# Optimization experiments

Hardware: AMD Instinct MI355X
Metric: run time of the kernel (lower is better)

## Reference

```python
import jax, jax.numpy as jnp
import numpy as np

D_MODEL = 2048
NUM_HEADS = 32
NUM_KV_HEADS = 8
D_K = D_MODEL // NUM_HEADS
B, S = 2, 2048


def setup_inputs() -> dict:
    key = jax.random.key(0)
    ks = jax.random.split(key, 6)
    sc = 1.0 / np.sqrt(D_MODEL)
    x = jax.random.normal(ks[0], (B, S, D_MODEL), dtype=jnp.float32)
    mask = jnp.tril(jnp.ones((S, S), dtype=jnp.float32))[None, None]  # [1,1,S,S]
    return {
        'x': x,
        'mask': mask,
        'Wq': jax.random.normal(ks[1], (D_MODEL, D_MODEL), jnp.float32) * sc,
        'bq': jnp.zeros((D_MODEL,), jnp.float32),
        'Wk': jax.random.normal(ks[2], (D_MODEL, NUM_KV_HEADS * D_K), jnp.float32) * sc,
        'bk': jnp.zeros((NUM_KV_HEADS * D_K,), jnp.float32),
        'Wv': jax.random.normal(ks[3], (D_MODEL, NUM_KV_HEADS * D_K), jnp.float32) * sc,
        'bv': jnp.zeros((NUM_KV_HEADS * D_K,), jnp.float32),
        'Wo': jax.random.normal(ks[4], (D_MODEL, D_MODEL), jnp.float32) * sc,
        'bo': jnp.zeros((D_MODEL,), jnp.float32),
    }


def reference(x, mask, Wq, bq, Wk, bk, Wv, bv, Wo, bo):
    b, s, _ = x.shape
    g = NUM_HEADS // NUM_KV_HEADS  # queries per kv head
    Q = (x @ Wq + bq).reshape(b, s, NUM_HEADS, D_K).transpose(0, 2, 1, 3)      # [b,h,s,dk]
    K = (x @ Wk + bk).reshape(b, s, NUM_KV_HEADS, D_K).transpose(0, 2, 1, 3)   # [b,kv,s,dk]
    V = (x @ Wv + bv).reshape(b, s, NUM_KV_HEADS, D_K).transpose(0, 2, 1, 3)
    # group queries per kv head instead of repeat_interleave on K/V
    Qg = Q.reshape(b, NUM_KV_HEADS, g, s, D_K)
    scores = jnp.einsum('bkgqd,bkld->bkgql', Qg, K) / np.sqrt(D_K)             # [b,kv,g,s,s]
    scores = jnp.where(mask[:, :, None] == 0, -1e9, scores)
    attn = jax.nn.softmax(scores, axis=-1)
    out = jnp.einsum('bkgql,bkld->bkgqd', attn, V)                              # [b,kv,g,s,dk]
    out = out.reshape(b, NUM_HEADS, s, D_K).transpose(0, 2, 1, 3).reshape(b, s, D_MODEL)
    return out @ Wo + bo
```

## Files before the change

kernel.cpp:

```cpp
#include <hip/hip_runtime.h>
#include <stdint.h>

typedef __bf16 bf16x8 __attribute__((ext_vector_type(8)));
typedef float  f32x4  __attribute__((ext_vector_type(4)));

__device__ __forceinline__ f32x4 mfma16(bf16x8 a, bf16x8 b, f32x4 c) {
    return __builtin_amdgcn_mfma_f32_16x16x32_bf16(a, b, c, 0, 0, 0);
}

__device__ __forceinline__ uint16_t f2bf(float f) {
    union { __bf16 b; uint16_t u; } cv; cv.b = (__bf16)f; return cv.u;
}

typedef __attribute__((address_space(3))) void as3_void;
typedef __attribute__((address_space(1))) void as1_void;
__device__ __forceinline__ void async_ld16(const void* g, void* l) {
    __builtin_amdgcn_global_load_lds((const as1_void*)g, (as3_void*)l, 16, 0, 0);
}


__global__ void convert_f32_bf16(const float* __restrict__ in, uint16_t* __restrict__ out, int n) {
    int i = (blockIdx.x * 256 + threadIdx.x) * 4;
    if (i >= n) return;
    float4 v = *(const float4*)(in + i);
    ushort4 o;
    o.x = f2bf(v.x); o.y = f2bf(v.y); o.z = f2bf(v.z); o.w = f2bf(v.w);
    *(ushort4*)(out + i) = o;
}

__global__ void transpose_f32_bf16(const float* __restrict__ in, uint16_t* __restrict__ out,
                                   int ldin, int out_off, int ldout) {
    __shared__ float tile[32][33];
    const int c0 = blockIdx.x << 5, r0 = blockIdx.y << 5;
    const int tx = threadIdx.x, ty = threadIdx.y;
#pragma unroll
    for (int i = 0; i < 4; ++i)
        tile[ty + i * 8][tx] = in[(size_t)(r0 + ty + i * 8) * ldin + c0 + tx];
    __syncthreads();
#pragma unroll
    for (int i = 0; i < 4; ++i)
        out[(size_t)(out_off + c0 + ty + i * 8) * ldout + r0 + tx] = f2bf(tile[tx][ty + i * 8]);
}

__global__ void transpose_v(const uint16_t* __restrict__ qkv, uint16_t* __restrict__ vt) {
    __shared__ uint16_t tile[32][33];
    const int c0 = blockIdx.x << 5, r0 = blockIdx.y << 5, b = blockIdx.z;
    const int tx = threadIdx.x, ty = threadIdx.y;
#pragma unroll
    for (int i = 0; i < 4; ++i)
        tile[ty + i * 8][tx] = qkv[(size_t)(b * 2048 + r0 + ty + i * 8) * 3072 + 2560 + c0 + tx];
    __syncthreads();
#pragma unroll
    for (int i = 0; i < 4; ++i)
        vt[(size_t)(b * 512 + c0 + ty + i * 8) * 2048 + r0 + tx] = tile[tx][ty + i * 8];
}

__global__ void concat_bias(const float* __restrict__ bq, const float* __restrict__ bk,
                            const float* __restrict__ bv, float* __restrict__ out) {
    int i = blockIdx.x * 256 + threadIdx.x;
    if (i >= 3072) return;
    out[i] = (i < 2048) ? bq[i] : (i < 2560 ? bk[i - 2048] : bv[i - 2560]);
}

template <bool F32OUT>
__global__ __launch_bounds__(256, 2)
void gemm_bt(const uint16_t* __restrict__ A, const uint16_t* __restrict__ Bt,
             const float* __restrict__ bias, void* __restrict__ Cout, int N, int K) {
    __shared__ __align__(16) uint16_t As[4096];
    __shared__ __align__(16) uint16_t Bs[4096];
    const int tid = threadIdx.x;
    const int wv = tid >> 6, ln = tid & 63;
    const int quad = ln >> 4, l16 = ln & 15;
    const int row0 = blockIdx.y << 7, col0 = blockIdx.x << 7;
    const int wm = wv >> 1, wn = wv & 1;

    const int p0 = tid, p1 = tid + 256;
    const int ar0 = p0 >> 2, ac0 = (p0 & 3) ^ ((ar0 ^ (ar0 >> 2)) & 3);
    const int ar1 = p1 >> 2, ac1 = (p1 & 3) ^ ((ar1 ^ (ar1 >> 2)) & 3);
    const uint16_t* gA0 = A + (size_t)(row0 + ar0) * K + (ac0 << 3);
    const uint16_t* gA1 = A + (size_t)(row0 + ar1) * K + (ac1 << 3);
    const uint16_t* gB0 = Bt + (size_t)(col0 + ar0) * K + (ac0 << 3);
    const uint16_t* gB1 = Bt + (size_t)(col0 + ar1) * K + (ac1 << 3);
    uint16_t* lA0 = As + (wv << 9);
    uint16_t* lA1 = As + 2048 + (wv << 9);
    uint16_t* lB0 = Bs + (wv << 9);
    uint16_t* lB1 = Bs + 2048 + (wv << 9);

    int a_off[4], b_off[4];
#pragma unroll
    for (int t = 0; t < 4; ++t) {
        int r = (wm << 6) + (t << 4) + l16;
        a_off[t] = (((r << 2) + (quad ^ ((r ^ (r >> 2)) & 3))) << 3);
        r = (wn << 6) + (t << 4) + l16;
        b_off[t] = (((r << 2) + (quad ^ ((r ^ (r >> 2)) & 3))) << 3);
    }

    f32x4 acc[4][4] = {};

    for (int k0 = 0; k0 < K; k0 += 32) {
        __syncthreads();
        async_ld16(gA0 + k0, lA0);
        async_ld16(gA1 + k0, lA1);
        async_ld16(gB0 + k0, lB0);
        async_ld16(gB1 + k0, lB1);
        __syncthreads();
        bf16x8 af[4], bfr[4];
#pragma unroll
        for (int t = 0; t < 4; ++t) af[t] = *(const bf16x8*)(As + a_off[t]);
#pragma unroll
        for (int t = 0; t < 4; ++t) bfr[t] = *(const bf16x8*)(Bs + b_off[t]);
#pragma unroll
        for (int mt = 0; mt < 4; ++mt)
#pragma unroll
            for (int nt = 0; nt < 4; ++nt)
                acc[mt][nt] = mfma16(af[mt], bfr[nt], acc[mt][nt]);
    }

#pragma unroll
    for (int nt = 0; nt < 4; ++nt) {
        const int col = col0 + (wn << 6) + (nt << 4) + l16;
        const float bv = bias[col];
#pragma unroll
        for (int mt = 0; mt < 4; ++mt) {
            const int rbase = row0 + (wm << 6) + (mt << 4) + (quad << 2);
#pragma unroll
            for (int r = 0; r < 4; ++r) {
                float v = acc[mt][nt][r] + bv;
                if (F32OUT)
                    ((float*)Cout)[(size_t)(rbase + r) * N + col] = v;
                else
                    ((uint16_t*)Cout)[(size_t)(rbase + r) * N + col] = f2bf(v);
            }
        }
    }
}

__global__ __launch_bounds__(128, 2)
void attn_fwd(const uint16_t* __restrict__ QKV, const uint16_t* __restrict__ Vt,
              uint16_t* __restrict__ AO) {
    __shared__ __align__(16) uint16_t Ks[2048];
    __shared__ __align__(16) uint16_t Vs[2048];
    __shared__ __align__(16) uint16_t Ps[2][1280];

    const int tid = threadIdx.x;
    const int wv = tid >> 6, ln = tid & 63;
    const int quad = ln >> 4, l16 = ln & 15;
    const int p = blockIdx.x, h = blockIdx.y, b = blockIdx.z;
    const int kvh = h >> 2;

    const uint16_t* Kg = QKV + (size_t)(b * 2048) * 3072 + 2048 + kvh * 64;
    const uint16_t* Vg = Vt + (size_t)(b * 512 + kvh * 64) * 2048;

    const int s0i = tid, s1i = tid + 128;
    const int kr0 = s0i >> 3, kc0 = (s0i & 7) ^ (kr0 & 7);
    const int kr1 = s1i >> 3, kc1 = (s1i & 7) ^ (kr1 & 7);
    const int vr0 = s0i >> 2, vc0 = (s0i & 3) ^ ((vr0 ^ (vr0 >> 2)) & 3);
    const int vr1 = s1i >> 2, vc1 = (s1i & 3) ^ ((vr1 ^ (vr1 >> 2)) & 3);

#pragma unroll
    for (int half = 0; half < 2; ++half) {
        const int t = half ? (31 - p) : p;
        const int q0 = t << 6;
        const int wq0 = q0 + (wv << 5);

        bf16x8 qf[2][2];
#pragma unroll
        for (int mt = 0; mt < 2; ++mt)
#pragma unroll
            for (int kk = 0; kk < 2; ++kk)
                qf[mt][kk] = *(const bf16x8*)(QKV +
                    (size_t)(b * 2048 + wq0 + mt * 16 + l16) * 3072 + h * 64 + kk * 32 + quad * 8);

        f32x4 acc[2][4] = {};
        float lpart[2][4] = {};

        const int nkb = 2 * t + 2;
        for (int kb = 0; kb < nkb; ++kb) {
            const int key0 = kb << 5;
            __syncthreads();
            *(uint4*)(Ks + s0i * 8) = *(const uint4*)(Kg + (size_t)(key0 + kr0) * 3072 + kc0 * 8);
            *(uint4*)(Ks + s1i * 8) = *(const uint4*)(Kg + (size_t)(key0 + kr1) * 3072 + kc1 * 8);
            *(uint4*)(Vs + s0i * 8) = *(const uint4*)(Vg + (size_t)vr0 * 2048 + key0 + vc0 * 8);
            *(uint4*)(Vs + s1i * 8) = *(const uint4*)(Vg + (size_t)vr1 * 2048 + key0 + vc1 * 8);
            __syncthreads();
            if (key0 > wq0 + 31) continue;

            bf16x8 kf[2][2];
#pragma unroll
            for (int nt = 0; nt < 2; ++nt)
#pragma unroll
                for (int kk = 0; kk < 2; ++kk) {
                    int r = nt * 16 + l16;
                    int c = kk * 4 + quad;
                    kf[nt][kk] = *(const bf16x8*)(Ks + ((r << 3) + (c ^ (r & 7))) * 8);
                }
            bf16x8 vf[4];
#pragma unroll
            for (int nt = 0; nt < 4; ++nt) {
                int r = nt * 16 + l16;
                vf[nt] = *(const bf16x8*)(Vs + (((r << 2) + (quad ^ ((r ^ (r >> 2)) & 3))) << 3));
            }

            const bool diag = (key0 + 31 > wq0);
#pragma unroll
            for (int mt = 0; mt < 2; ++mt) {
                f32x4 s0 = {0.f, 0.f, 0.f, 0.f}, s1 = {0.f, 0.f, 0.f, 0.f};
                s0 = mfma16(qf[mt][0], kf[0][0], s0);
                s0 = mfma16(qf[mt][1], kf[0][1], s0);
                s1 = mfma16(qf[mt][0], kf[1][0], s1);
                s1 = mfma16(qf[mt][1], kf[1][1], s1);
#pragma unroll
                for (int r = 0; r < 4; ++r) {
                    float e0 = __expf(fmaf(s0[r], 0.125f, -16.0f));
                    float e1 = __expf(fmaf(s1[r], 0.125f, -16.0f));
                    if (diag) {
                        const int qrow = wq0 + mt * 16 + quad * 4 + r;
                        if (key0 + l16 > qrow) e0 = 0.0f;
                        if (key0 + 16 + l16 > qrow) e1 = 0.0f;
                    }
                    lpart[mt][r] += e0 + e1;
                    const int prow = mt * 16 + quad * 4 + r;
                    Ps[wv][prow * 40 + l16] = f2bf(e0);
                    Ps[wv][prow * 40 + 16 + l16] = f2bf(e1);
                }
            }
#pragma unroll
            for (int mt = 0; mt < 2; ++mt) {
                bf16x8 pf = *(const bf16x8*)(&Ps[wv][(mt * 16 + l16) * 40 + quad * 8]);
#pragma unroll
                for (int nt = 0; nt < 4; ++nt)
                    acc[mt][nt] = mfma16(pf, vf[nt], acc[mt][nt]);
            }
        }

#pragma unroll
        for (int mt = 0; mt < 2; ++mt) {
            float inv[4];
#pragma unroll
            for (int r = 0; r < 4; ++r) {
                float rs = lpart[mt][r];
#pragma unroll
                for (int off = 1; off < 16; off <<= 1)
                    rs += __shfl_xor(rs, off, 64);
                inv[r] = 1.0f / rs;
            }
#pragma unroll
            for (int nt = 0; nt < 4; ++nt)
#pragma unroll
                for (int r = 0; r < 4; ++r) {
                    const int qrow = wq0 + mt * 16 + quad * 4 + r;
                    AO[(size_t)(b * 2048 + qrow) * 2048 + h * 64 + nt * 16 + l16] =
                        f2bf(acc[mt][nt][r] * inv[r]);
                }
        }
    }
}


extern "C" void kernel_launch(void* const* d_in, const int* in_sizes, int n_in,
                              void* d_out, int out_size, void* d_ws, size_t ws_size,
                              hipStream_t stream) {
    (void)in_sizes; (void)n_in; (void)out_size; (void)ws_size;
    const float* x  = (const float*)d_in[0];
    const float* Wq = (const float*)d_in[2];
    const float* bq = (const float*)d_in[3];
    const float* Wk = (const float*)d_in[4];
    const float* bk = (const float*)d_in[5];
    const float* Wv = (const float*)d_in[6];
    const float* bv = (const float*)d_in[7];
    const float* Wo = (const float*)d_in[8];
    const float* bo = (const float*)d_in[9];

    char* ws = (char*)d_ws;
    uint16_t* xb    = (uint16_t*)ws;
    uint16_t* wqkvT = (uint16_t*)(ws + 16777216);
    uint16_t* woT   = (uint16_t*)(ws + 16777216 + 12582912);
    float*    biasq = (float*)(ws + 16777216 + 12582912 + 8388608);
    uint16_t* qkv   = (uint16_t*)d_out;
    uint16_t* ao    = xb;
    uint16_t* vt    = wqkvT;

    dim3 tb(32, 8);
    convert_f32_bf16<<<8192, 256, 0, stream>>>(x, xb, 4096 * 2048);
    transpose_f32_bf16<<<dim3(64, 64), tb, 0, stream>>>(Wq, wqkvT, 2048, 0,    2048);
    transpose_f32_bf16<<<dim3(16, 64), tb, 0, stream>>>(Wk, wqkvT, 512,  2048, 2048);
    transpose_f32_bf16<<<dim3(16, 64), tb, 0, stream>>>(Wv, wqkvT, 512,  2560, 2048);
    transpose_f32_bf16<<<dim3(64, 64), tb, 0, stream>>>(Wo, woT,   2048, 0,    2048);
    concat_bias<<<12, 256, 0, stream>>>(bq, bk, bv, biasq);

    gemm_bt<false><<<dim3(24, 32), 256, 0, stream>>>(xb, wqkvT, biasq, qkv, 3072, 2048);
    transpose_v<<<dim3(16, 64, 2), tb, 0, stream>>>(qkv, vt);
    attn_fwd<<<dim3(16, 32, 2), 128, 0, stream>>>(qkv, vt, ao);
    gemm_bt<true><<<dim3(16, 32), 256, 0, stream>>>(ao, woT, bo, d_out, 2048, 2048);
}
```

Measured before the change: 342.8 us.

## Share K/V tiles across GQA heads per block with async double-buffered loads

```diff
diff --git a/kernel.cpp b/kernel.cpp
--- a/kernel.cpp
+++ b/kernel.cpp
@@ -135,33 +135,45 @@
     }
 }
 
-__global__ __launch_bounds__(128, 2)
+__global__ __launch_bounds__(256, 2)
 void attn_fwd(const uint16_t* __restrict__ QKV, const uint16_t* __restrict__ Vt,
               uint16_t* __restrict__ AO) {
-    __shared__ __align__(16) uint16_t Ks[2048];
-    __shared__ __align__(16) uint16_t Vs[2048];
-    __shared__ __align__(16) uint16_t Ps[2][1280];
+    __shared__ __align__(16) uint16_t Ks[2][2048];
+    __shared__ __align__(16) uint16_t Vs[2][2048];
+    __shared__ __align__(16) uint16_t Ps[4][1280];
 
     const int tid = threadIdx.x;
     const int wv = tid >> 6, ln = tid & 63;
     const int quad = ln >> 4, l16 = ln & 15;
-    const int p = blockIdx.x, h = blockIdx.y, b = blockIdx.z;
-    const int kvh = h >> 2;
+    const int p = blockIdx.x, kvh = blockIdx.y, b = blockIdx.z;
+    const int h = kvh * 4 + wv;
 
     const uint16_t* Kg = QKV + (size_t)(b * 2048) * 3072 + 2048 + kvh * 64;
     const uint16_t* Vg = Vt + (size_t)(b * 512 + kvh * 64) * 2048;
 
-    const int s0i = tid, s1i = tid + 128;
-    const int kr0 = s0i >> 3, kc0 = (s0i & 7) ^ (kr0 & 7);
-    const int kr1 = s1i >> 3, kc1 = (s1i & 7) ^ (kr1 & 7);
-    const int vr0 = s0i >> 2, vc0 = (s0i & 3) ^ ((vr0 ^ (vr0 >> 2)) & 3);
-    const int vr1 = s1i >> 2, vc1 = (s1i & 3) ^ ((vr1 ^ (vr1 >> 2)) & 3);
+    const int kr = tid >> 3, kc = (tid & 7) ^ (kr & 7);
+    const int vr = tid >> 2, vc = (tid & 3) ^ ((vr ^ (vr >> 2)) & 3);
+    const uint16_t* KgT = Kg + (size_t)kr * 3072 + kc * 8;
+    const uint16_t* VgT = Vg + (size_t)vr * 2048 + vc * 8;
+
+    int kf_off[2][2], vf_off[4];
+#pragma unroll
+    for (int nt = 0; nt < 2; ++nt)
+#pragma unroll
+        for (int kk = 0; kk < 2; ++kk) {
+            int r = nt * 16 + l16, c = kk * 4 + quad;
+            kf_off[nt][kk] = ((r << 3) + (c ^ (r & 7))) << 3;
+        }
+#pragma unroll
+    for (int nt = 0; nt < 4; ++nt) {
+        int r = nt * 16 + l16;
+        vf_off[nt] = ((r << 2) + (quad ^ ((r ^ (r >> 2)) & 3))) << 3;
+    }
 
 #pragma unroll
     for (int half = 0; half < 2; ++half) {
-        const int t = half ? (31 - p) : p;
-        const int q0 = t << 6;
-        const int wq0 = q0 + (wv << 5);
+        const int w = half ? (63 - p) : p;
+        const int q0 = w << 5;
 
         bf16x8 qf[2][2];
 #pragma unroll
@@ -169,39 +181,37 @@
 #pragma unroll
             for (int kk = 0; kk < 2; ++kk)
                 qf[mt][kk] = *(const bf16x8*)(QKV +
-                    (size_t)(b * 2048 + wq0 + mt * 16 + l16) * 3072 + h * 64 + kk * 32 + quad * 8);
+                    (size_t)(b * 2048 + q0 + mt * 16 + l16) * 3072 + h * 64 + kk * 32 + quad * 8);
 
         f32x4 acc[2][4] = {};
         float lpart[2][4] = {};
 
-        const int nkb = 2 * t + 2;
+        const int nkb = w + 1;
+        __syncthreads();
+        async_ld16(KgT, Ks[0] + (wv << 9));
+        async_ld16(VgT, Vs[0] + (wv << 9));
+
         for (int kb = 0; kb < nkb; ++kb) {
+            const int cur = kb & 1;
             const int key0 = kb << 5;
             __syncthreads();
-            *(uint4*)(Ks + s0i * 8) = *(const uint4*)(Kg + (size_t)(key0 + kr0) * 3072 + kc0 * 8);
-            *(uint4*)(Ks + s1i * 8) = *(const uint4*)(Kg + (size_t)(key0 + kr1) * 3072 + kc1 * 8);
-            *(uint4*)(Vs + s0i * 8) = *(const uint4*)(Vg + (size_t)vr0 * 2048 + key0 + vc0 * 8);
-            *(uint4*)(Vs + s1i * 8) = *(const uint4*)(Vg + (size_t)vr1 * 2048 + key0 + vc1 * 8);
-            __syncthreads();
-            if (key0 > wq0 + 31) continue;
+            if (kb + 1 < nkb) {
+                async_ld16(KgT + ((kb + 1) << 5) * 3072, Ks[cur ^ 1] + (wv << 9));
+                async_ld16(VgT + ((kb + 1) << 5), Vs[cur ^ 1] + (wv << 9));
+            }
 
             bf16x8 kf[2][2];
 #pragma unroll
             for (int nt = 0; nt < 2; ++nt)
 #pragma unroll
-                for (int kk = 0; kk < 2; ++kk) {
-                    int r = nt * 16 + l16;
-                    int c = kk * 4 + quad;
-                    kf[nt][kk] = *(const bf16x8*)(Ks + ((r << 3) + (c ^ (r & 7))) * 8);
-                }
+                for (int kk = 0; kk < 2; ++kk)
+                    kf[nt][kk] = *(const bf16x8*)(Ks[cur] + kf_off[nt][kk]);
             bf16x8 vf[4];
 #pragma unroll
-            for (int nt = 0; nt < 4; ++nt) {
-                int r = nt * 16 + l16;
-                vf[nt] = *(const bf16x8*)(Vs + (((r << 2) + (quad ^ ((r ^ (r >> 2)) & 3))) << 3));
-            }
-
-            const bool diag = (key0 + 31 > wq0);
+            for (int nt = 0; nt < 4; ++nt)
+                vf[nt] = *(const bf16x8*)(Vs[cur] + vf_off[nt]);
+
+            const bool diag = (kb == nkb - 1);
 #pragma unroll
             for (int mt = 0; mt < 2; ++mt) {
                 f32x4 s0 = {0.f, 0.f, 0.f, 0.f}, s1 = {0.f, 0.f, 0.f, 0.f};
@@ -214,7 +224,7 @@
                     float e0 = __expf(fmaf(s0[r], 0.125f, -16.0f));
                     float e1 = __expf(fmaf(s1[r], 0.125f, -16.0f));
                     if (diag) {
-                        const int qrow = wq0 + mt * 16 + quad * 4 + r;
+                        const int qrow = q0 + mt * 16 + quad * 4 + r;
                         if (key0 + l16 > qrow) e0 = 0.0f;
                         if (key0 + 16 + l16 > qrow) e1 = 0.0f;
                     }
@@ -248,7 +258,7 @@
             for (int nt = 0; nt < 4; ++nt)
 #pragma unroll
                 for (int r = 0; r < 4; ++r) {
-                    const int qrow = wq0 + mt * 16 + quad * 4 + r;
+                    const int qrow = q0 + mt * 16 + quad * 4 + r;
                     AO[(size_t)(b * 2048 + qrow) * 2048 + h * 64 + nt * 16 + l16] =
                         f2bf(acc[mt][nt][r] * inv[r]);
                 }
@@ -290,6 +300,6 @@
 
     gemm_bt<false><<<dim3(24, 32), 256, 0, stream>>>(xb, wqkvT, biasq, qkv, 3072, 2048);
     transpose_v<<<dim3(16, 64, 2), tb, 0, stream>>>(qkv, vt);
-    attn_fwd<<<dim3(16, 32, 2), 128, 0, stream>>>(qkv, vt, ao);
+    attn_fwd<<<dim3(32, 8, 2), 256, 0, stream>>>(qkv, vt, ao);
     gemm_bt<true><<<dim3(16, 32), 256, 0, stream>>>(ao, woT, bo, d_out, 2048, 2048);
 }
```

New measurement: 329.2 us. 1.04x faster.
